# Optimization experiments

Measured on AMD Instinct MI355X. Metric: run time of the kernel, lower is better.

Reference implementation:

```python
import jax, jax.numpy as jnp
import numpy as np

B, L, D_MODEL, N_HEADS = 2, 2048, 2048, 16
HALF = D_MODEL // 2            # 1024
HD = HALF // N_HEADS           # 64 (head dim actually used by the reshape)
SCALE = float(np.sqrt(D_MODEL / N_HEADS))  # sqrt(128), per source's self.scale
EPS = 1e-5


def setup_inputs() -> dict:
    key = jax.random.key(0)
    ks = jax.random.split(key, 12)
    s = 1.0 / np.sqrt(HALF)
    d = dict(
        x_a=jax.random.normal(ks[0], (B, L, HALF), jnp.float32),
        x_b=jax.random.normal(ks[1], (B, L, HALF), jnp.float32),
        Wq_a=jax.random.normal(ks[2], (HALF, HALF), jnp.float32) * s,
        Wq_b=jax.random.normal(ks[3], (HALF, HALF), jnp.float32) * s,
        Wk_a=jax.random.normal(ks[4], (HALF, HALF), jnp.float32) * s,
        Wk_b=jax.random.normal(ks[5], (HALF, HALF), jnp.float32) * s,
        Wv_a=jax.random.normal(ks[6], (HALF, HALF), jnp.float32) * s,
        Wv_b=jax.random.normal(ks[7], (HALF, HALF), jnp.float32) * s,
        Wo_a=jax.random.normal(ks[8], (HALF, HALF), jnp.float32) * s,
        Wo_b=jax.random.normal(ks[9], (HALF, HALF), jnp.float32) * s,
        gamma_a=jnp.ones((HALF,), jnp.float32),
        beta_a=jnp.zeros((HALF,), jnp.float32),
        gamma_b=jnp.ones((HALF,), jnp.float32),
        beta_b=jnp.zeros((HALF,), jnp.float32),
    )
    return d


def _heads(x, W):
    # torch Linear (no bias): x @ W.T, then split heads -> (B, H, L, HD)
    y = jnp.einsum('bld,ed->ble', x, W)
    Bb, Ll, _ = y.shape
    return y.reshape(Bb, Ll, N_HEADS, HD).transpose(0, 2, 1, 3)


def _ln(x, gamma, beta):
    mu = jnp.mean(x, axis=-1, keepdims=True)
    var = jnp.var(x, axis=-1, keepdims=True)
    return (x - mu) * jax.lax.rsqrt(var + EPS) * gamma + beta


def reference(x_a, x_b, Wq_a, Wq_b, Wk_a, Wk_b, Wv_a, Wv_b, Wo_a, Wo_b,
              gamma_a, beta_a, gamma_b, beta_b):
    q_a = _heads(x_a, Wq_a); k_a = _heads(x_a, Wk_a); v_a = _heads(x_a, Wv_a)
    q_b = _heads(x_b, Wq_b); k_b = _heads(x_b, Wk_b); v_b = _heads(x_b, Wv_b)

    # cross-attention: branch a attends over branch b and vice versa
    scores_a = jnp.einsum('bhqd,bhkd->bhqk', q_a, k_b) / SCALE
    scores_b = jnp.einsum('bhqd,bhkd->bhqk', q_b, k_a) / SCALE
    w_a = jax.nn.softmax(scores_a, axis=-1)
    w_b = jax.nn.softmax(scores_b, axis=-1)

    o_a = jnp.einsum('bhqk,bhkd->bhqd', w_a, v_b)
    o_b = jnp.einsum('bhqk,bhkd->bhqd', w_b, v_a)
    o_a = o_a.transpose(0, 2, 1, 3).reshape(x_a.shape)
    o_b = o_b.transpose(0, 2, 1, 3).reshape(x_b.shape)

    o_a = jnp.einsum('bld,ed->ble', o_a, Wo_a)
    o_b = jnp.einsum('bld,ed->ble', o_b, Wo_b)

    y_a = _ln(x_a + o_a, gamma_a, beta_a)
    y_b = _ln(x_b + o_b, gamma_b, beta_b)
    return y_a, y_b
```

## Files before the change

### kernel.cpp

```cpp
#include <hip/hip_runtime.h>
#include <cstdint>
#include <cstddef>

typedef __bf16 bf16x8 __attribute__((ext_vector_type(8)));
typedef float f32x4 __attribute__((ext_vector_type(4)));
typedef unsigned short u16x8 __attribute__((ext_vector_type(8)));
typedef unsigned short u16x4 __attribute__((ext_vector_type(4)));
typedef short s16x4 __attribute__((ext_vector_type(4)));
typedef unsigned short u16;

#define L_SEQ 2048
#define D_HALF 1024
#define HDIM 64
static constexpr float EXP2_SCALE = 0.12751742552639395f;

__device__ inline u16 f2b(float f) {
  uint32_t u; __builtin_memcpy(&u, &f, 4);
  u = u + 0x7FFFu + ((u >> 16) & 1u);
  return (u16)(u >> 16);
}

__device__ inline uint32_t cvt_pk_bf16(float lo, float hi) {
  uint32_t r;
  asm("v_cvt_pk_bf16_f32 %0, %1, %2" : "=v"(r) : "v"(lo), "v"(hi));
  return r;
}

__global__ __launch_bounds__(256)
void convx(const float* xa, const float* xb, u16* dst) {
  const float* s = blockIdx.y ? xb : xa;
  size_t i = ((size_t)blockIdx.x * 256 + threadIdx.x) * 8;
  float4 v0 = *(const float4*)(s + i);
  float4 v1 = *(const float4*)(s + i + 4);
  u16x8 p;
  p[0] = f2b(v0.x); p[1] = f2b(v0.y); p[2] = f2b(v0.z); p[3] = f2b(v0.w);
  p[4] = f2b(v1.x); p[5] = f2b(v1.y); p[6] = f2b(v1.z); p[7] = f2b(v1.w);
  *(u16x8*)&dst[(size_t)blockIdx.y * 4194304 + i] = p;
}

struct CArg8 { const float* src[8]; };
__global__ __launch_bounds__(256)
void convw8(CArg8 a, u16* dst) {
  const int z = blockIdx.y;
  const float* s = a.src[z];
  size_t i = ((size_t)blockIdx.x * 256 + threadIdx.x) * 8;
  float4 v0 = *(const float4*)(s + i);
  float4 v1 = *(const float4*)(s + i + 4);
  u16x8 p;
  p[0] = f2b(v0.x); p[1] = f2b(v0.y); p[2] = f2b(v0.z); p[3] = f2b(v0.w);
  p[4] = f2b(v1.x); p[5] = f2b(v1.y); p[6] = f2b(v1.z); p[7] = f2b(v1.w);
  *(u16x8*)&dst[(size_t)z * 1048576 + i] = p;
}

struct GArg { const u16* A; const u16* W; u16* C; const float* R; float* Z; int vt; };
struct GArgs { GArg g[6]; };

template <bool RESID>
__global__ __launch_bounds__(256, 2)
void gemm_nt(GArgs args, int M, int N, int K) {
  GArg ga = args.g[blockIdx.z];
  __shared__ __attribute__((aligned(16))) u16 As[128][72];
  __shared__ __attribute__((aligned(16))) u16 Bs[128][72];

  const int tid = threadIdx.x;
  const int wv = tid >> 6, lane = tid & 63;
  const int lane15 = lane & 15, quad = lane >> 4;
  const int m0 = blockIdx.y * 128, n0 = blockIdx.x * 128;
  const int wm = (wv >> 1) * 64, wn = (wv & 1) * 64;

  int rr[4], cc[4];
#pragma unroll
  for (int i = 0; i < 4; i++) { int c = tid + i * 256; rr[i] = c >> 3; cc[i] = (c & 7) * 8; }

  u16x8 ra[4], rb[4];
#pragma unroll
  for (int i = 0; i < 4; i++) {
    ra[i] = *(const u16x8*)&ga.A[(size_t)(m0 + rr[i]) * K + cc[i]];
    rb[i] = *(const u16x8*)&ga.W[(size_t)(n0 + rr[i]) * K + cc[i]];
  }

  f32x4 acc[4][4] = {};

  for (int k0 = 0; k0 < K; k0 += 64) {
    __syncthreads();
#pragma unroll
    for (int i = 0; i < 4; i++) {
      *(u16x8*)&As[rr[i]][cc[i]] = ra[i];
      *(u16x8*)&Bs[rr[i]][cc[i]] = rb[i];
    }
    if (k0 + 64 < K) {
#pragma unroll
      for (int i = 0; i < 4; i++) {
        ra[i] = *(const u16x8*)&ga.A[(size_t)(m0 + rr[i]) * K + k0 + 64 + cc[i]];
        rb[i] = *(const u16x8*)&ga.W[(size_t)(n0 + rr[i]) * K + k0 + 64 + cc[i]];
      }
    }
    __syncthreads();
#pragma unroll
    for (int kk = 0; kk < 64; kk += 32) {
      bf16x8 af[4], bw[4];
#pragma unroll
      for (int i = 0; i < 4; i++)
        af[i] = *(const bf16x8*)&As[wm + i * 16 + lane15][kk + quad * 8];
#pragma unroll
      for (int j = 0; j < 4; j++)
        bw[j] = *(const bf16x8*)&Bs[wn + j * 16 + lane15][kk + quad * 8];
#pragma unroll
      for (int i = 0; i < 4; i++)
#pragma unroll
        for (int j = 0; j < 4; j++)
          acc[i][j] = __builtin_amdgcn_mfma_f32_16x16x32_bf16(af[i], bw[j], acc[i][j], 0, 0, 0);
    }
  }

  if (!RESID && ga.vt) {
#pragma unroll
    for (int i = 0; i < 4; i++)
#pragma unroll
      for (int j = 0; j < 4; j++) {
        int gm0 = m0 + wm + i * 16 + quad * 4;
        int gn  = n0 + wn + j * 16 + lane15;
        int bb = gm0 >> 11, t = gm0 & 2047;
        u16x4 pk;
#pragma unroll
        for (int r = 0; r < 4; r++) pk[r] = f2b(acc[i][j][r]);
        *(u16x4*)&ga.C[(size_t)bb * 2097152 + (size_t)gn * 2048 + t] = pk;
      }
  } else {
#pragma unroll
    for (int i = 0; i < 4; i++)
#pragma unroll
      for (int j = 0; j < 4; j++)
#pragma unroll
        for (int r = 0; r < 4; r++) {
          int gm = m0 + wm + i * 16 + quad * 4 + r;
          int gn = n0 + wn + j * 16 + lane15;
          size_t idx = (size_t)gm * N + gn;
          if (RESID) ga.Z[idx] = acc[i][j][r] + ga.R[idx];
          else       ga.C[idx] = f2b(acc[i][j][r]);
        }
  }
}

#if __has_builtin(__builtin_amdgcn_mfma_f32_16x16x16bf16_1k)
#define HAVE_MFMA16 1
#else
#define HAVE_MFMA16 0
#endif

__global__ __launch_bounds__(256, 2)
void attn_kernel(const u16* q_a, const u16* k_a, const u16* vt_a,
                 const u16* q_b, const u16* k_b, const u16* vt_b,
                 u16* o_a, u16* o_b) {
  const int br = blockIdx.z;
  const u16* Q  = br ? q_b : q_a;
  const u16* Kp = br ? k_a : k_b;
  const u16* Vp = br ? vt_a : vt_b;
  u16* O = br ? o_b : o_a;
  const int bh = blockIdx.y;
  const int b = bh >> 4, h = bh & 15;
  const int q0 = blockIdx.x * 128;

  const int tid = threadIdx.x, wv = tid >> 6, lane = tid & 63;
  const int lane15 = lane & 15, quad = lane >> 4;

  __shared__ __attribute__((aligned(16))) u16 Ks[2][64][72];
  __shared__ __attribute__((aligned(16))) u16 Vt[2][64][72];
#if !HAVE_MFMA16
  __shared__ __attribute__((aligned(16))) u16 Pw[4][2][16][72];
#endif

  const size_t base   = ((size_t)b * L_SEQ) * D_HALF + (size_t)h * HDIM;
  const size_t vbase  = (size_t)b * 2097152 + (size_t)(h * 64) * 2048;

  const int c1 = tid + 256;
  const int r0 = tid >> 3, cb0 = (tid & 7) * 8;
  const int r1 = c1 >> 3,  cb1 = (c1 & 7) * 8;

  bf16x8 qf[2][2];
#pragma unroll
  for (int f = 0; f < 2; f++) {
    const int qrow = q0 + wv * 32 + f * 16 + lane15;
#pragma unroll
    for (int c = 0; c < 2; c++)
      qf[f][c] = *(const bf16x8*)&Q[base + (size_t)qrow * D_HALF + c * 32 + quad * 8];
  }

  u16x8 kr0 = *(const u16x8*)&Kp[base + (size_t)r0 * D_HALF + cb0];
  u16x8 kr1 = *(const u16x8*)&Kp[base + (size_t)r1 * D_HALF + cb1];
  u16x8 vr0 = *(const u16x8*)&Vp[vbase + (size_t)r0 * 2048 + cb0];
  u16x8 vr1 = *(const u16x8*)&Vp[vbase + (size_t)r1 * 2048 + cb1];
  *(u16x8*)&Ks[0][r0][cb0] = kr0;
  *(u16x8*)&Ks[0][r1][cb1] = kr1;
  *(u16x8*)&Vt[0][r0][cb0] = vr0;
  *(u16x8*)&Vt[0][r1][cb1] = vr1;
  __syncthreads();

  f32x4 oacc[2][4] = {};
  float lsum[2] = {0.f, 0.f};

  for (int it = 0; it < 32; it++) {
    const int cur = it & 1, nxt = cur ^ 1;
    if (it < 31) {
      const int kt = (it + 1) * 64;
      kr0 = *(const u16x8*)&Kp[base + (size_t)(kt + r0) * D_HALF + cb0];
      kr1 = *(const u16x8*)&Kp[base + (size_t)(kt + r1) * D_HALF + cb1];
      vr0 = *(const u16x8*)&Vp[vbase + (size_t)r0 * 2048 + kt + cb0];
      vr1 = *(const u16x8*)&Vp[vbase + (size_t)r1 * 2048 + kt + cb1];
    }

    f32x4 s[2][4];
#pragma unroll
    for (int nt = 0; nt < 4; nt++) {
      bf16x8 kb0 = *(const bf16x8*)&Ks[cur][nt * 16 + lane15][quad * 8];
      bf16x8 kb1 = *(const bf16x8*)&Ks[cur][nt * 16 + lane15][32 + quad * 8];
#pragma unroll
      for (int f = 0; f < 2; f++) {
        f32x4 a0 = {};
        a0 = __builtin_amdgcn_mfma_f32_16x16x32_bf16(kb0, qf[f][0], a0, 0, 0, 0);
        a0 = __builtin_amdgcn_mfma_f32_16x16x32_bf16(kb1, qf[f][1], a0, 0, 0, 0);
        s[f][nt] = a0;
      }
    }

    s16x4 pa[2][4];
#pragma unroll
    for (int f = 0; f < 2; f++)
#pragma unroll
      for (int nt = 0; nt < 4; nt++) {
        float p0 = __builtin_amdgcn_exp2f(s[f][nt][0] * EXP2_SCALE);
        float p1 = __builtin_amdgcn_exp2f(s[f][nt][1] * EXP2_SCALE);
        float p2 = __builtin_amdgcn_exp2f(s[f][nt][2] * EXP2_SCALE);
        float p3 = __builtin_amdgcn_exp2f(s[f][nt][3] * EXP2_SCALE);
        lsum[f] += (p0 + p1) + (p2 + p3);
        union { uint32_t u[2]; s16x4 v; } cv;
        cv.u[0] = cvt_pk_bf16(p0, p1);
        cv.u[1] = cvt_pk_bf16(p2, p3);
        pa[f][nt] = cv.v;
      }

#if HAVE_MFMA16
#pragma unroll
    for (int dt = 0; dt < 4; dt++) {
      s16x4 bv[4];
#pragma unroll
      for (int nt = 0; nt < 4; nt++)
        bv[nt] = *(const s16x4*)&Vt[cur][dt * 16 + lane15][nt * 16 + quad * 4];
#pragma unroll
      for (int f = 0; f < 2; f++) {
        f32x4 t = oacc[f][dt];
#pragma unroll
        for (int nt = 0; nt < 4; nt++)
          t = __builtin_amdgcn_mfma_f32_16x16x16bf16_1k(pa[f][nt], bv[nt], t, 0, 0, 0);
        oacc[f][dt] = t;
      }
    }
#else
#pragma unroll
    for (int f = 0; f < 2; f++)
#pragma unroll
      for (int nt = 0; nt < 4; nt++)
        *(s16x4*)&Pw[wv][f][lane15][nt * 16 + quad * 4] = pa[f][nt];
    __asm__ volatile("s_waitcnt lgkmcnt(0)" ::: "memory");
    bf16x8 pb[2][2];
#pragma unroll
    for (int f = 0; f < 2; f++) {
      pb[f][0] = *(const bf16x8*)&Pw[wv][f][lane15][quad * 8];
      pb[f][1] = *(const bf16x8*)&Pw[wv][f][lane15][32 + quad * 8];
    }
#pragma unroll
    for (int dt = 0; dt < 4; dt++) {
      bf16x8 bv0 = *(const bf16x8*)&Vt[cur][dt * 16 + lane15][quad * 8];
      bf16x8 bv1 = *(const bf16x8*)&Vt[cur][dt * 16 + lane15][32 + quad * 8];
#pragma unroll
      for (int f = 0; f < 2; f++) {
        f32x4 t = oacc[f][dt];
        t = __builtin_amdgcn_mfma_f32_16x16x32_bf16(pb[f][0], bv0, t, 0, 0, 0);
        t = __builtin_amdgcn_mfma_f32_16x16x32_bf16(pb[f][1], bv1, t, 0, 0, 0);
        oacc[f][dt] = t;
      }
    }
    __asm__ volatile("" ::: "memory");
#endif

    if (it < 31) {
      *(u16x8*)&Ks[nxt][r0][cb0] = kr0;
      *(u16x8*)&Ks[nxt][r1][cb1] = kr1;
      *(u16x8*)&Vt[nxt][r0][cb0] = vr0;
      *(u16x8*)&Vt[nxt][r1][cb1] = vr1;
    }
    __syncthreads();
  }

#pragma unroll
  for (int f = 0; f < 2; f++) {
    float lt = lsum[f];
    lt += __shfl_xor(lt, 16);
    lt += __shfl_xor(lt, 32);
    lsum[f] = lt;
  }
#pragma unroll
  for (int f = 0; f < 2; f++) {
    float linv[4];
#pragma unroll
    for (int r = 0; r < 4; r++)
      linv[r] = 1.0f / __shfl(lsum[f], quad * 4 + r);
#pragma unroll
    for (int dt = 0; dt < 4; dt++)
#pragma unroll
      for (int r = 0; r < 4; r++) {
        float val = oacc[f][dt][r] * linv[r];
        O[base + (size_t)(q0 + wv * 32 + f * 16 + quad * 4 + r) * D_HALF
          + dt * 16 + lane15] = f2b(val);
      }
  }
}

__global__ __launch_bounds__(256)
void ln_kernel(const float* zA, const float* zB,
               const float* gA, const float* bA, const float* gB, const float* bB,
               float* out) {
  const int row = blockIdx.x, br = blockIdx.y;
  const float* z = (br ? zB : zA) + (size_t)row * D_HALF;
  const float* g  = br ? gB : gA;
  const float* be = br ? bB : bA;
  float* o = out + (size_t)br * ((size_t)4096 * D_HALF) + (size_t)row * D_HALF;

  float4 v = ((const float4*)z)[threadIdx.x];
  float s  = v.x + v.y + v.z + v.w;
  float s2 = v.x * v.x + v.y * v.y + v.z * v.z + v.w * v.w;
#pragma unroll
  for (int off = 32; off > 0; off >>= 1) {
    s  += __shfl_down(s, off);
    s2 += __shfl_down(s2, off);
  }
  __shared__ float red[8];
  int w = threadIdx.x >> 6, ln = threadIdx.x & 63;
  if (ln == 0) { red[w] = s; red[4 + w] = s2; }
  __syncthreads();
  if (threadIdx.x == 0) {
    red[0] = red[0] + red[1] + red[2] + red[3];
    red[4] = red[4] + red[5] + red[6] + red[7];
  }
  __syncthreads();
  float mu  = red[0] * (1.0f / 1024.0f);
  float var = red[4] * (1.0f / 1024.0f) - mu * mu;
  float rs  = rsqrtf(fmaxf(var, 0.0f) + 1e-5f);

  int col = threadIdx.x * 4;
  float4 gv = ((const float4*)g)[threadIdx.x];
  float4 bv = ((const float4*)be)[threadIdx.x];
  float4 ov;
  ov.x = (v.x - mu) * rs * gv.x + bv.x;
  ov.y = (v.y - mu) * rs * gv.y + bv.y;
  ov.z = (v.z - mu) * rs * gv.z + bv.z;
  ov.w = (v.w - mu) * rs * gv.w + bv.w;
  *(float4*)&o[col] = ov;
}

extern "C" void kernel_launch(void* const* d_in, const int* in_sizes, int n_in,
                              void* d_out, int out_size, void* d_ws, size_t ws_size,
                              hipStream_t stream) {
  const float* x_a     = (const float*)d_in[0];
  const float* x_b     = (const float*)d_in[1];
  const float* Wq_a    = (const float*)d_in[2];
  const float* Wq_b    = (const float*)d_in[3];
  const float* Wk_a    = (const float*)d_in[4];
  const float* Wk_b    = (const float*)d_in[5];
  const float* Wv_a    = (const float*)d_in[6];
  const float* Wv_b    = (const float*)d_in[7];
  const float* Wo_a    = (const float*)d_in[8];
  const float* Wo_b    = (const float*)d_in[9];
  const float* gamma_a = (const float*)d_in[10];
  const float* beta_a  = (const float*)d_in[11];
  const float* gamma_b = (const float*)d_in[12];
  const float* beta_b  = (const float*)d_in[13];

  const size_t BUF = (size_t)4096 * 1024;
  u16* ws   = (u16*)d_ws;
  u16* q_a  = ws + 0 * BUF; u16* k_a  = ws + 1 * BUF; u16* vt_a = ws + 2 * BUF;
  u16* q_b  = ws + 3 * BUF; u16* k_b  = ws + 4 * BUF; u16* vt_b = ws + 5 * BUF;
  u16* wall = ws + 6 * BUF;
  float* z_a = (float*)(ws + 0 * BUF);
  float* z_b = (float*)(ws + 2 * BUF);

  u16* xbf_a = (u16*)d_out;
  u16* xbf_b = xbf_a + 4194304;
  u16* o_a   = (u16*)d_out;
  u16* o_b   = o_a + 4194304;

  const int M = 4096, N = 1024, K = 1024;

  convx<<<dim3(2048, 2), 256, 0, stream>>>(x_a, x_b, xbf_a);

  CArg8 cw;
  cw.src[0] = Wq_a; cw.src[1] = Wk_a; cw.src[2] = Wv_a;
  cw.src[3] = Wq_b; cw.src[4] = Wk_b; cw.src[5] = Wv_b;
  cw.src[6] = Wo_a; cw.src[7] = Wo_b;
  convw8<<<dim3(512, 8), 256, 0, stream>>>(cw, wall);

  GArgs qkv;
  qkv.g[0] = GArg{xbf_a, wall + 0 * 1048576, q_a,  nullptr, nullptr, 0};
  qkv.g[1] = GArg{xbf_a, wall + 1 * 1048576, k_a,  nullptr, nullptr, 0};
  qkv.g[2] = GArg{xbf_a, wall + 2 * 1048576, vt_a, nullptr, nullptr, 1};
  qkv.g[3] = GArg{xbf_b, wall + 3 * 1048576, q_b,  nullptr, nullptr, 0};
  qkv.g[4] = GArg{xbf_b, wall + 4 * 1048576, k_b,  nullptr, nullptr, 0};
  qkv.g[5] = GArg{xbf_b, wall + 5 * 1048576, vt_b, nullptr, nullptr, 1};
  gemm_nt<false><<<dim3(8, 32, 6), 256, 0, stream>>>(qkv, M, N, K);

  attn_kernel<<<dim3(16, 32, 2), 256, 0, stream>>>(q_a, k_a, vt_a, q_b, k_b, vt_b, o_a, o_b);

  GArgs op;
  op.g[0] = GArg{o_a, wall + 6 * 1048576, nullptr, x_a, z_a, 0};
  op.g[1] = GArg{o_b, wall + 7 * 1048576, nullptr, x_b, z_b, 0};
  op.g[2] = op.g[0]; op.g[3] = op.g[0]; op.g[4] = op.g[0]; op.g[5] = op.g[0];
  gemm_nt<true><<<dim3(8, 32, 2), 256, 0, stream>>>(op, M, N, K);

  ln_kernel<<<dim3(4096, 2), 256, 0, stream>>>(z_a, z_b, gamma_a, beta_a,
                                               gamma_b, beta_b, (float*)d_out);
}
```

Before: 341.6 us.

## Use direct global-to-LDS loads with XOR swizzle, fold softmax scale into Q projection

The GEMM now streams tiles straight into double-buffered, XOR-swizzled LDS with global_load_lds, removing the register staging step and one barrier per K step. The attention kernel replaces padded LDS rows with an XOR-swizzled layout and raises wave priority around the MFMA phases. The exp2 softmax scale is folded into the Q projection epilogue, so the per-element multiply in the attention loop goes away. The non-MFMA16 fallback path is removed. Rounding Q to bf16 after scaling slightly changes numerics, and the LDS ordering of the async loads relies on the existing barriers.

```diff
diff --git a/kernel.cpp b/kernel.cpp
--- a/kernel.cpp
+++ b/kernel.cpp
@@ -25,6 +25,10 @@
   asm("v_cvt_pk_bf16_f32 %0, %1, %2" : "=v"(r) : "v"(lo), "v"(hi));
   return r;
 }
+
+#define GLOAD16(gp, lp) __builtin_amdgcn_global_load_lds( \
+    (const __attribute__((address_space(1))) unsigned int*)(gp), \
+    (__attribute__((address_space(3))) unsigned int*)(lp), 16, 0, 0)
 
 __global__ __launch_bounds__(256)
 void convx(const float* xa, const float* xb, u16* dst) {
@@ -52,15 +56,16 @@
   *(u16x8*)&dst[(size_t)z * 1048576 + i] = p;
 }
 
-struct GArg { const u16* A; const u16* W; u16* C; const float* R; float* Z; int vt; };
+struct GArg { const u16* A; const u16* W; u16* C; const float* R; float* Z;
+              int vt; float alpha; };
 struct GArgs { GArg g[6]; };
 
 template <bool RESID>
 __global__ __launch_bounds__(256, 2)
 void gemm_nt(GArgs args, int M, int N, int K) {
   GArg ga = args.g[blockIdx.z];
-  __shared__ __attribute__((aligned(16))) u16 As[128][72];
-  __shared__ __attribute__((aligned(16))) u16 Bs[128][72];
+  __shared__ __attribute__((aligned(16))) u16 As[2][8192];
+  __shared__ __attribute__((aligned(16))) u16 Bs[2][8192];
 
   const int tid = threadIdx.x;
   const int wv = tid >> 6, lane = tid & 63;
@@ -68,43 +73,49 @@
   const int m0 = blockIdx.y * 128, n0 = blockIdx.x * 128;
   const int wm = (wv >> 1) * 64, wn = (wv & 1) * 64;
 
-  int rr[4], cc[4];
-#pragma unroll
-  for (int i = 0; i < 4; i++) { int c = tid + i * 256; rr[i] = c >> 3; cc[i] = (c & 7) * 8; }
-
-  u16x8 ra[4], rb[4];
-#pragma unroll
-  for (int i = 0; i < 4; i++) {
-    ra[i] = *(const u16x8*)&ga.A[(size_t)(m0 + rr[i]) * K + cc[i]];
-    rb[i] = *(const u16x8*)&ga.W[(size_t)(n0 + rr[i]) * K + cc[i]];
+  const int srow = lane >> 3;
+  const int scol = ((lane & 7) ^ srow) * 8;
+
+  const u16* pA[4]; const u16* pW[4]; int lo[4];
+#pragma unroll
+  for (int j = 0; j < 4; j++) {
+    int r = wv * 32 + j * 8;
+    pA[j] = ga.A + (size_t)(m0 + r + srow) * K + scol;
+    pW[j] = ga.W + (size_t)(n0 + r + srow) * K + scol;
+    lo[j] = r * 64;
   }
 
   f32x4 acc[4][4] = {};
+  const int swz = (lane15 & 7) << 4;
+
+#pragma unroll
+  for (int j = 0; j < 4; j++) {
+    GLOAD16(pA[j], &As[0][lo[j]]);
+    GLOAD16(pW[j], &Bs[0][lo[j]]);
+  }
 
   for (int k0 = 0; k0 < K; k0 += 64) {
+    const int cur = (k0 >> 6) & 1;
     __syncthreads();
-#pragma unroll
-    for (int i = 0; i < 4; i++) {
-      *(u16x8*)&As[rr[i]][cc[i]] = ra[i];
-      *(u16x8*)&Bs[rr[i]][cc[i]] = rb[i];
-    }
     if (k0 + 64 < K) {
 #pragma unroll
-      for (int i = 0; i < 4; i++) {
-        ra[i] = *(const u16x8*)&ga.A[(size_t)(m0 + rr[i]) * K + k0 + 64 + cc[i]];
-        rb[i] = *(const u16x8*)&ga.W[(size_t)(n0 + rr[i]) * K + k0 + 64 + cc[i]];
-      }
-    }
-    __syncthreads();
-#pragma unroll
-    for (int kk = 0; kk < 64; kk += 32) {
+      for (int j = 0; j < 4; j++) {
+        GLOAD16(pA[j] + k0 + 64, &As[cur ^ 1][lo[j]]);
+        GLOAD16(pW[j] + k0 + 64, &Bs[cur ^ 1][lo[j]]);
+      }
+    }
+    const char* ab = (const char*)As[cur];
+    const char* bb = (const char*)Bs[cur];
+#pragma unroll
+    for (int kk = 0; kk < 2; kk++) {
+      const int cb = kk * 64 + quad * 16;
       bf16x8 af[4], bw[4];
 #pragma unroll
       for (int i = 0; i < 4; i++)
-        af[i] = *(const bf16x8*)&As[wm + i * 16 + lane15][kk + quad * 8];
+        af[i] = *(const bf16x8*)(ab + (wm + i * 16 + lane15) * 128 + (cb ^ swz));
 #pragma unroll
       for (int j = 0; j < 4; j++)
-        bw[j] = *(const bf16x8*)&Bs[wn + j * 16 + lane15][kk + quad * 8];
+        bw[j] = *(const bf16x8*)(bb + (wn + j * 16 + lane15) * 128 + (cb ^ swz));
 #pragma unroll
       for (int i = 0; i < 4; i++)
 #pragma unroll
@@ -113,6 +124,7 @@
     }
   }
 
+  const float al = ga.alpha;
   if (!RESID && ga.vt) {
 #pragma unroll
     for (int i = 0; i < 4; i++)
@@ -120,11 +132,11 @@
       for (int j = 0; j < 4; j++) {
         int gm0 = m0 + wm + i * 16 + quad * 4;
         int gn  = n0 + wn + j * 16 + lane15;
-        int bb = gm0 >> 11, t = gm0 & 2047;
+        int bb2 = gm0 >> 11, t = gm0 & 2047;
         u16x4 pk;
 #pragma unroll
-        for (int r = 0; r < 4; r++) pk[r] = f2b(acc[i][j][r]);
-        *(u16x4*)&ga.C[(size_t)bb * 2097152 + (size_t)gn * 2048 + t] = pk;
+        for (int r = 0; r < 4; r++) pk[r] = f2b(acc[i][j][r] * al);
+        *(u16x4*)&ga.C[(size_t)bb2 * 2097152 + (size_t)gn * 2048 + t] = pk;
       }
   } else {
 #pragma unroll
@@ -137,16 +149,12 @@
           int gn = n0 + wn + j * 16 + lane15;
           size_t idx = (size_t)gm * N + gn;
           if (RESID) ga.Z[idx] = acc[i][j][r] + ga.R[idx];
-          else       ga.C[idx] = f2b(acc[i][j][r]);
+          else       ga.C[idx] = f2b(acc[i][j][r] * al);
         }
   }
 }
 
-#if __has_builtin(__builtin_amdgcn_mfma_f32_16x16x16bf16_1k)
-#define HAVE_MFMA16 1
-#else
-#define HAVE_MFMA16 0
-#endif
+#define SWZ(row, bcol) ((row) * 128 + ((bcol) ^ (((row) & 7) << 4)))
 
 __global__ __launch_bounds__(256, 2)
 void attn_kernel(const u16* q_a, const u16* k_a, const u16* vt_a,
@@ -164,18 +172,16 @@
   const int tid = threadIdx.x, wv = tid >> 6, lane = tid & 63;
   const int lane15 = lane & 15, quad = lane >> 4;
 
-  __shared__ __attribute__((aligned(16))) u16 Ks[2][64][72];
-  __shared__ __attribute__((aligned(16))) u16 Vt[2][64][72];
-#if !HAVE_MFMA16
-  __shared__ __attribute__((aligned(16))) u16 Pw[4][2][16][72];
-#endif
+  __shared__ __attribute__((aligned(16))) u16 Ks[2][4096];
+  __shared__ __attribute__((aligned(16))) u16 Vt[2][4096];
 
   const size_t base   = ((size_t)b * L_SEQ) * D_HALF + (size_t)h * HDIM;
   const size_t vbase  = (size_t)b * 2097152 + (size_t)(h * 64) * 2048;
 
   const int c1 = tid + 256;
-  const int r0 = tid >> 3, cb0 = (tid & 7) * 8;
-  const int r1 = c1 >> 3,  cb1 = (c1 & 7) * 8;
+  const int r0 = tid >> 3, cb0 = (tid & 7) * 16;
+  const int r1 = c1 >> 3,  cb1 = (c1 & 7) * 16;
+  const int wo0 = SWZ(r0, cb0), wo1 = SWZ(r1, cb1);
 
   bf16x8 qf[2][2];
 #pragma unroll
@@ -186,34 +192,40 @@
       qf[f][c] = *(const bf16x8*)&Q[base + (size_t)qrow * D_HALF + c * 32 + quad * 8];
   }
 
-  u16x8 kr0 = *(const u16x8*)&Kp[base + (size_t)r0 * D_HALF + cb0];
-  u16x8 kr1 = *(const u16x8*)&Kp[base + (size_t)r1 * D_HALF + cb1];
-  u16x8 vr0 = *(const u16x8*)&Vp[vbase + (size_t)r0 * 2048 + cb0];
-  u16x8 vr1 = *(const u16x8*)&Vp[vbase + (size_t)r1 * 2048 + cb1];
-  *(u16x8*)&Ks[0][r0][cb0] = kr0;
-  *(u16x8*)&Ks[0][r1][cb1] = kr1;
-  *(u16x8*)&Vt[0][r0][cb0] = vr0;
-  *(u16x8*)&Vt[0][r1][cb1] = vr1;
+  u16x8 kr0 = *(const u16x8*)&Kp[base + (size_t)r0 * D_HALF + cb0 / 2];
+  u16x8 kr1 = *(const u16x8*)&Kp[base + (size_t)r1 * D_HALF + cb1 / 2];
+  u16x8 vr0 = *(const u16x8*)&Vp[vbase + (size_t)r0 * 2048 + cb0 / 2];
+  u16x8 vr1 = *(const u16x8*)&Vp[vbase + (size_t)r1 * 2048 + cb1 / 2];
+  *(u16x8*)((char*)Ks[0] + wo0) = kr0;
+  *(u16x8*)((char*)Ks[0] + wo1) = kr1;
+  *(u16x8*)((char*)Vt[0] + wo0) = vr0;
+  *(u16x8*)((char*)Vt[0] + wo1) = vr1;
   __syncthreads();
 
   f32x4 oacc[2][4] = {};
   float lsum[2] = {0.f, 0.f};
+  const int aswz = (lane15 & 7) << 4;
 
   for (int it = 0; it < 32; it++) {
     const int cur = it & 1, nxt = cur ^ 1;
     if (it < 31) {
       const int kt = (it + 1) * 64;
-      kr0 = *(const u16x8*)&Kp[base + (size_t)(kt + r0) * D_HALF + cb0];
-      kr1 = *(const u16x8*)&Kp[base + (size_t)(kt + r1) * D_HALF + cb1];
-      vr0 = *(const u16x8*)&Vp[vbase + (size_t)r0 * 2048 + kt + cb0];
-      vr1 = *(const u16x8*)&Vp[vbase + (size_t)r1 * 2048 + kt + cb1];
-    }
+      kr0 = *(const u16x8*)&Kp[base + (size_t)(kt + r0) * D_HALF + cb0 / 2];
+      kr1 = *(const u16x8*)&Kp[base + (size_t)(kt + r1) * D_HALF + cb1 / 2];
+      vr0 = *(const u16x8*)&Vp[vbase + (size_t)r0 * 2048 + kt + cb0 / 2];
+      vr1 = *(const u16x8*)&Vp[vbase + (size_t)r1 * 2048 + kt + cb1 / 2];
+    }
+
+    const char* kb = (const char*)Ks[cur];
+    const char* vb = (const char*)Vt[cur];
 
     f32x4 s[2][4];
+    __builtin_amdgcn_s_setprio(1);
 #pragma unroll
     for (int nt = 0; nt < 4; nt++) {
-      bf16x8 kb0 = *(const bf16x8*)&Ks[cur][nt * 16 + lane15][quad * 8];
-      bf16x8 kb1 = *(const bf16x8*)&Ks[cur][nt * 16 + lane15][32 + quad * 8];
+      const int krow = nt * 16 + lane15;
+      bf16x8 kb0 = *(const bf16x8*)(kb + SWZ(krow, quad * 16));
+      bf16x8 kb1 = *(const bf16x8*)(kb + SWZ(krow, 64 + quad * 16));
 #pragma unroll
       for (int f = 0; f < 2; f++) {
         f32x4 a0 = {};
@@ -222,16 +234,17 @@
         s[f][nt] = a0;
       }
     }
+    __builtin_amdgcn_s_setprio(0);
 
     s16x4 pa[2][4];
 #pragma unroll
     for (int f = 0; f < 2; f++)
 #pragma unroll
       for (int nt = 0; nt < 4; nt++) {
-        float p0 = __builtin_amdgcn_exp2f(s[f][nt][0] * EXP2_SCALE);
-        float p1 = __builtin_amdgcn_exp2f(s[f][nt][1] * EXP2_SCALE);
-        float p2 = __builtin_amdgcn_exp2f(s[f][nt][2] * EXP2_SCALE);
-        float p3 = __builtin_amdgcn_exp2f(s[f][nt][3] * EXP2_SCALE);
+        float p0 = __builtin_amdgcn_exp2f(s[f][nt][0]);
+        float p1 = __builtin_amdgcn_exp2f(s[f][nt][1]);
+        float p2 = __builtin_amdgcn_exp2f(s[f][nt][2]);
+        float p3 = __builtin_amdgcn_exp2f(s[f][nt][3]);
         lsum[f] += (p0 + p1) + (p2 + p3);
         union { uint32_t u[2]; s16x4 v; } cv;
         cv.u[0] = cvt_pk_bf16(p0, p1);
@@ -239,13 +252,14 @@
         pa[f][nt] = cv.v;
       }
 
-#if HAVE_MFMA16
+    __builtin_amdgcn_s_setprio(1);
 #pragma unroll
     for (int dt = 0; dt < 4; dt++) {
+      const int vrow = dt * 16 + lane15;
       s16x4 bv[4];
 #pragma unroll
       for (int nt = 0; nt < 4; nt++)
-        bv[nt] = *(const s16x4*)&Vt[cur][dt * 16 + lane15][nt * 16 + quad * 4];
+        bv[nt] = *(const s16x4*)(vb + SWZ(vrow, nt * 32 + quad * 8));
 #pragma unroll
       for (int f = 0; f < 2; f++) {
         f32x4 t = oacc[f][dt];
@@ -255,39 +269,13 @@
         oacc[f][dt] = t;
       }
     }
-#else
-#pragma unroll
-    for (int f = 0; f < 2; f++)
-#pragma unroll
-      for (int nt = 0; nt < 4; nt++)
-        *(s16x4*)&Pw[wv][f][lane15][nt * 16 + quad * 4] = pa[f][nt];
-    __asm__ volatile("s_waitcnt lgkmcnt(0)" ::: "memory");
-    bf16x8 pb[2][2];
-#pragma unroll
-    for (int f = 0; f < 2; f++) {
-      pb[f][0] = *(const bf16x8*)&Pw[wv][f][lane15][quad * 8];
-      pb[f][1] = *(const bf16x8*)&Pw[wv][f][lane15][32 + quad * 8];
-    }
-#pragma unroll
-    for (int dt = 0; dt < 4; dt++) {
-      bf16x8 bv0 = *(const bf16x8*)&Vt[cur][dt * 16 + lane15][quad * 8];
-      bf16x8 bv1 = *(const bf16x8*)&Vt[cur][dt * 16 + lane15][32 + quad * 8];
-#pragma unroll
-      for (int f = 0; f < 2; f++) {
-        f32x4 t = oacc[f][dt];
-        t = __builtin_amdgcn_mfma_f32_16x16x32_bf16(pb[f][0], bv0, t, 0, 0, 0);
-        t = __builtin_amdgcn_mfma_f32_16x16x32_bf16(pb[f][1], bv1, t, 0, 0, 0);
-        oacc[f][dt] = t;
-      }
-    }
-    __asm__ volatile("" ::: "memory");
-#endif
+    __builtin_amdgcn_s_setprio(0);
 
     if (it < 31) {
-      *(u16x8*)&Ks[nxt][r0][cb0] = kr0;
-      *(u16x8*)&Ks[nxt][r1][cb1] = kr1;
-      *(u16x8*)&Vt[nxt][r0][cb0] = vr0;
-      *(u16x8*)&Vt[nxt][r1][cb1] = vr1;
+      *(u16x8*)((char*)Ks[nxt] + wo0) = kr0;
+      *(u16x8*)((char*)Ks[nxt] + wo1) = kr1;
+      *(u16x8*)((char*)Vt[nxt] + wo0) = vr0;
+      *(u16x8*)((char*)Vt[nxt] + wo1) = vr1;
     }
     __syncthreads();
   }
@@ -400,19 +388,19 @@
   convw8<<<dim3(512, 8), 256, 0, stream>>>(cw, wall);
 
   GArgs qkv;
-  qkv.g[0] = GArg{xbf_a, wall + 0 * 1048576, q_a,  nullptr, nullptr, 0};
-  qkv.g[1] = GArg{xbf_a, wall + 1 * 1048576, k_a,  nullptr, nullptr, 0};
-  qkv.g[2] = GArg{xbf_a, wall + 2 * 1048576, vt_a, nullptr, nullptr, 1};
-  qkv.g[3] = GArg{xbf_b, wall + 3 * 1048576, q_b,  nullptr, nullptr, 0};
-  qkv.g[4] = GArg{xbf_b, wall + 4 * 1048576, k_b,  nullptr, nullptr, 0};
-  qkv.g[5] = GArg{xbf_b, wall + 5 * 1048576, vt_b, nullptr, nullptr, 1};
+  qkv.g[0] = GArg{xbf_a, wall + 0 * 1048576, q_a,  nullptr, nullptr, 0, EXP2_SCALE};
+  qkv.g[1] = GArg{xbf_a, wall + 1 * 1048576, k_a,  nullptr, nullptr, 0, 1.0f};
+  qkv.g[2] = GArg{xbf_a, wall + 2 * 1048576, vt_a, nullptr, nullptr, 1, 1.0f};
+  qkv.g[3] = GArg{xbf_b, wall + 3 * 1048576, q_b,  nullptr, nullptr, 0, EXP2_SCALE};
+  qkv.g[4] = GArg{xbf_b, wall + 4 * 1048576, k_b,  nullptr, nullptr, 0, 1.0f};
+  qkv.g[5] = GArg{xbf_b, wall + 5 * 1048576, vt_b, nullptr, nullptr, 1, 1.0f};
   gemm_nt<false><<<dim3(8, 32, 6), 256, 0, stream>>>(qkv, M, N, K);
 
   attn_kernel<<<dim3(16, 32, 2), 256, 0, stream>>>(q_a, k_a, vt_a, q_b, k_b, vt_b, o_a, o_b);
 
   GArgs op;
-  op.g[0] = GArg{o_a, wall + 6 * 1048576, nullptr, x_a, z_a, 0};
-  op.g[1] = GArg{o_b, wall + 7 * 1048576, nullptr, x_b, z_b, 0};
+  op.g[0] = GArg{o_a, wall + 6 * 1048576, nullptr, x_a, z_a, 0, 1.0f};
+  op.g[1] = GArg{o_b, wall + 7 * 1048576, nullptr, x_b, z_b, 0, 1.0f};
   op.g[2] = op.g[0]; op.g[3] = op.g[0]; op.g[4] = op.g[0]; op.g[5] = op.g[0];
   gemm_nt<true><<<dim3(8, 32, 2), 256, 0, stream>>>(op, M, N, K);
 
```

Result: no change. 340.3 us (-0.4%).
